# Kernel optimization log

Measured on AMD Instinct MI355X. Metric: run time of the kernel, lower is better.

The kernel has to match this reference:

```python
import jax, jax.numpy as jnp
import numpy as np
import math

D_MODEL = 1024
NUM_HEADS = 16
D_FF = 4096
EPS = 1e-5


def _linear_params(key, fan_in, fan_out):
    # torch nn.Linear default init: U(-1/sqrt(fan_in), 1/sqrt(fan_in))
    k1, k2 = jax.random.split(key)
    bound = 1.0 / math.sqrt(fan_in)
    W = jax.random.uniform(k1, (fan_in, fan_out), jnp.float32, -bound, bound)
    b = jax.random.uniform(k2, (fan_out,), jnp.float32, -bound, bound)
    return W, b


def setup_inputs() -> dict:
    key = jax.random.key(0)
    keys = jax.random.split(key, 16)
    src = jax.random.normal(keys[0], (4, 2048, D_MODEL), jnp.float32)
    tgt = jax.random.normal(keys[1], (4, 2048, D_MODEL), jnp.float32)
    sa_wq, sa_bq = _linear_params(keys[2], D_MODEL, D_MODEL)
    sa_wk, sa_bk = _linear_params(keys[3], D_MODEL, D_MODEL)
    sa_wv, sa_bv = _linear_params(keys[4], D_MODEL, D_MODEL)
    sa_wo, sa_bo = _linear_params(keys[5], D_MODEL, D_MODEL)
    ca_wq, ca_bq = _linear_params(keys[6], D_MODEL, D_MODEL)
    ca_wk, ca_bk = _linear_params(keys[7], D_MODEL, D_MODEL)
    ca_wv, ca_bv = _linear_params(keys[8], D_MODEL, D_MODEL)
    ca_wo, ca_bo = _linear_params(keys[9], D_MODEL, D_MODEL)
    ff_w1, ff_b1 = _linear_params(keys[10], D_MODEL, D_FF)
    ff_w2, ff_b2 = _linear_params(keys[11], D_FF, D_MODEL)
    ones = jnp.ones((D_MODEL,), jnp.float32)
    zeros = jnp.zeros((D_MODEL,), jnp.float32)
    return dict(
        src=src, tgt=tgt,
        sa_wq=sa_wq, sa_bq=sa_bq, sa_wk=sa_wk, sa_bk=sa_bk,
        sa_wv=sa_wv, sa_bv=sa_bv, sa_wo=sa_wo, sa_bo=sa_bo,
        ca_wq=ca_wq, ca_bq=ca_bq, ca_wk=ca_wk, ca_bk=ca_bk,
        ca_wv=ca_wv, ca_bv=ca_bv, ca_wo=ca_wo, ca_bo=ca_bo,
        ff_w1=ff_w1, ff_b1=ff_b1, ff_w2=ff_w2, ff_b2=ff_b2,
        ln1_g=ones, ln1_b=zeros, ln2_g=ones, ln2_b=zeros,
        ln3_g=ones, ln3_b=zeros,
    )


def _layernorm(x, g, b):
    mu = jnp.mean(x, axis=-1, keepdims=True)
    var = jnp.mean((x - mu) ** 2, axis=-1, keepdims=True)
    return (x - mu) * jax.lax.rsqrt(var + EPS) * g + b


def _mha(q_in, kv_in, wq, bq, wk, bk, wv, bv, wo, bo):
    B, Sq, D = q_in.shape
    Skv = kv_in.shape[1]
    H, dk = NUM_HEADS, D // NUM_HEADS
    Q = (q_in @ wq + bq).reshape(B, Sq, H, dk).transpose(0, 2, 1, 3)
    K = (kv_in @ wk + bk).reshape(B, Skv, H, dk).transpose(0, 2, 1, 3)
    V = (kv_in @ wv + bv).reshape(B, Skv, H, dk).transpose(0, 2, 1, 3)
    scores = jnp.einsum('bhqd,bhkd->bhqk', Q, K) / math.sqrt(dk)
    probs = jax.nn.softmax(scores, axis=-1)
    attn = jnp.einsum('bhqk,bhkd->bhqd', probs, V)
    attn = attn.transpose(0, 2, 1, 3).reshape(B, Sq, D)
    return attn @ wo + bo


def reference(src, tgt,
              sa_wq, sa_bq, sa_wk, sa_bk, sa_wv, sa_bv, sa_wo, sa_bo,
              ca_wq, ca_bq, ca_wk, ca_bk, ca_wv, ca_bv, ca_wo, ca_bo,
              ff_w1, ff_b1, ff_w2, ff_b2,
              ln1_g, ln1_b, ln2_g, ln2_b, ln3_g, ln3_b):
    # self-attention on tgt (dropout = identity in eval)
    sa = _mha(tgt, tgt, sa_wq, sa_bq, sa_wk, sa_bk, sa_wv, sa_bv, sa_wo, sa_bo)
    x = _layernorm(tgt + sa, ln1_g, ln1_b)
    # cross-attention: queries from decoder, keys/values from src
    ca = _mha(x, src, ca_wq, ca_bq, ca_wk, ca_bk, ca_wv, ca_bv, ca_wo, ca_bo)
    x = _layernorm(x + ca, ln2_g, ln2_b)
    # feed-forward
    ff = jax.nn.relu(x @ ff_w1 + ff_b1) @ ff_w2 + ff_b2
    x = _layernorm(x + ff, ln3_g, ln3_b)
    return x
```

## Files before the change

kernel.cpp:

```cpp
#include <hip/hip_runtime.h>
#include <hip/hip_bf16.h>
#include <stdint.h>


typedef __bf16 bf16_t;
typedef __bf16 bf16x8 __attribute__((ext_vector_type(8)));
typedef __bf16 bf16x4 __attribute__((ext_vector_type(4)));
typedef float  f32x4  __attribute__((ext_vector_type(4)));
typedef short  s16x4  __attribute__((ext_vector_type(4)));

#define SEQ_    2048
#define BATCH_  4
#define DM_     1024
#define NH_     16
#define DK_     64
#define DFF_    4096
#define TOK_    (BATCH_*SEQ_)
#define BH_     (BATCH_*NH_)
#define HEADEL_ ((size_t)BH_*SEQ_*DK_)

#define QSCALE_ 0.18033688011112042f

#define MFMA_BF16(a,b,c) __builtin_amdgcn_mfma_f32_16x16x32_bf16((a),(b),(c),0,0,0)
#define MFMA16(a,b,c) __builtin_amdgcn_mfma_f32_16x16x16bf16_1k((a),(b),(c),0,0,0)

static __device__ __forceinline__ void gl_lds16(const void* g, void* l) {
  __builtin_amdgcn_global_load_lds(
      (const __attribute__((address_space(1))) uint32_t*)g,
      (__attribute__((address_space(3))) uint32_t*)l, 16, 0, 0);
}

static __device__ __forceinline__ float fast_exp2(float x) {
#if __has_builtin(__builtin_amdgcn_exp2f)
  return __builtin_amdgcn_exp2f(x);
#else
  return exp2f(x);
#endif
}

__global__ __launch_bounds__(256) void cvt_bf16(const float* __restrict__ in,
                                                bf16_t* __restrict__ out, int n4) {
  int i = blockIdx.x * 256 + threadIdx.x;
  if (i < n4) {
    f32x4 v = *(const f32x4*)(in + (size_t)i * 4);
    bf16x4 o;
    o[0] = (bf16_t)v[0]; o[1] = (bf16_t)v[1]; o[2] = (bf16_t)v[2]; o[3] = (bf16_t)v[3];
    *(bf16x4*)(out + (size_t)i * 4) = o;
  }
}

__global__ __launch_bounds__(256) void transpose_w(const float* __restrict__ W,
                                                   bf16_t* __restrict__ Wt,
                                                   int K, int N) {
  __shared__ float t[32][33];
  int bx = blockIdx.x * 32;
  int by = blockIdx.y * 32;
  int tx = threadIdx.x;
  int ty = threadIdx.y;
  #pragma unroll
  for (int i = 0; i < 32; i += 8)
    t[ty + i][tx] = W[(size_t)(by + ty + i) * N + bx + tx];
  __syncthreads();
  #pragma unroll
  for (int i = 0; i < 32; i += 8)
    Wt[(size_t)(bx + ty + i) * K + by + tx] = (bf16_t)t[tx][ty + i];
}

__global__ __launch_bounds__(256) void gemm_bf16(
    const bf16_t* __restrict__ A, const bf16_t* __restrict__ Bt,
    const float* __restrict__ bias, const float* __restrict__ bias2,
    const float* __restrict__ bias3,
    float* outF, bf16_t* outB,
    int M, int N, int K, int mode, int relu, float scale)
{
  __shared__ __attribute__((aligned(16))) bf16_t lsA[2][128 * 32];
  __shared__ __attribute__((aligned(16))) bf16_t lsB[2][128 * 32];

  const int tid  = threadIdx.x;
  const int lane = tid & 63;
  const int w    = tid >> 6;
  const int q    = lane >> 4;
  const int r    = lane & 15;

  const int gx = gridDim.x;
  const int b  = blockIdx.y * gx + blockIdx.x;
  const int t_ = b >> 3;
  const int bm = (t_ / gx) * 8 + (b & 7);
  const int bn = t_ % gx;
  const int m0 = bm * 128;
  const int n0 = bn * 128;

  const int mb   = (w >> 1) * 64;
  const int nb   = (w & 1) * 64;

  f32x4 acc[4][4] = {};

  const int srow = tid >> 3;
  const int scol = (tid & 7) * 8 + 0;

  for (int k0 = 0; k0 < K; k0 += 64) {
    #pragma unroll
    for (int h = 0; h < 2; ++h) {
      #pragma unroll
      for (int rr = 0; rr < 2; ++rr) {
        int flat = rr * 2048 + tid * 8;
        int row = flat >> 5, col = flat & 31;
        gl_lds16(A  + (size_t)(m0 + row) * K + k0 + 32 * h + col, &lsA[h][flat]);
        gl_lds16(Bt + (size_t)(n0 + row) * K + k0 + 32 * h + col, &lsB[h][flat]);
      }
    }
    __syncthreads();
    #pragma unroll
    for (int h = 0; h < 2; ++h) {
      bf16x8 af[4], bfr[4];
      #pragma unroll
      for (int mi = 0; mi < 4; ++mi)
        af[mi] = *(const bf16x8*)&lsA[h][(mb + mi * 16 + r) * 32 + q * 8];
      #pragma unroll
      for (int ni = 0; ni < 4; ++ni)
        bfr[ni] = *(const bf16x8*)&lsB[h][(nb + ni * 16 + r) * 32 + q * 8];
      #pragma unroll
      for (int mi = 0; mi < 4; ++mi)
        #pragma unroll
        for (int ni = 0; ni < 4; ++ni)
          acc[mi][ni] = MFMA_BF16(af[mi], bfr[ni], acc[mi][ni]);
    }
    __syncthreads();
  }

  #pragma unroll
  for (int mi = 0; mi < 4; ++mi) {
    #pragma unroll
    for (int ni = 0; ni < 4; ++ni) {
      int col = n0 + nb + ni * 16 + r;
      float bv, sc = scale;
      int seg = 0, cw = col;
      if (mode == 3) {
        seg = col >> 10; cw = col & 1023;
        bv = (seg == 0) ? bias[cw] : ((seg == 1) ? bias2[cw] : bias3[cw]);
        if (seg != 0) sc = 1.f;
      } else if (mode == 4) {
        seg = col >> 10; cw = col & 1023;
        bv = (seg == 0) ? bias[cw] : bias2[cw];
      } else {
        bv = bias[col];
      }
      #pragma unroll
      for (int i = 0; i < 4; ++i) {
        int row = m0 + mb + mi * 16 + q * 4 + i;
        float v = (acc[mi][ni][i] + bv) * sc;
        if (relu) v = fmaxf(v, 0.f);
        if (outF) outF[(size_t)row * N + col] = v;
        if (outB) {
          size_t idx;
          if (mode == 0) {
            idx = (size_t)row * N + col;
          } else {
            int bb = row >> 11, s = row & 2047, h = cw >> 6, d = cw & 63;
            bool vt;
            size_t base;
            if (mode == 1)      { vt = false; base = 0; }
            else if (mode == 2) { vt = true;  base = 0; }
            else if (mode == 3) { vt = (seg == 2); base = (size_t)seg * HEADEL_; }
            else                { vt = (seg == 1); base = (size_t)seg * HEADEL_; }
            if (!vt) idx = base + ((size_t)(bb * NH_ + h) * SEQ_ + s) * DK_ + d;
            else     idx = base + ((size_t)(bb * NH_ + h) * DK_ + d) * SEQ_ + s;
          }
          outB[idx] = (bf16_t)v;
        }
      }
    }
  }
}

__global__ __launch_bounds__(256) void flash_attn(
    const bf16_t* __restrict__ Q, const bf16_t* __restrict__ Kb,
    const bf16_t* __restrict__ Vt, bf16_t* __restrict__ O)
{
  __shared__ __attribute__((aligned(16))) bf16_t Kls[64 * 64];
  __shared__ __attribute__((aligned(16))) bf16_t Vls[64 * 64];

  const int tid  = threadIdx.x;
  const int w    = tid >> 6;
  const int lane = tid & 63;
  const int q    = lane >> 4;
  const int r    = lane & 15;

  const int bl   = blockIdx.y * gridDim.x + blockIdx.x;
  const int bh   = (bl & 7) * 8 + ((bl >> 3) & 7);
  const int q0   = (bl >> 6) * 128 + w * 32;

  const bf16_t* Qp  = Q  + ((size_t)bh * SEQ_ + q0) * DK_;
  const bf16_t* Kp0 = Kb + (size_t)bh * SEQ_ * DK_;
  const bf16_t* Vp0 = Vt + (size_t)bh * DK_ * SEQ_;

  bf16x8 aq[2][2];
  #pragma unroll
  for (int rt = 0; rt < 2; ++rt)
    #pragma unroll
    for (int c = 0; c < 2; ++c)
      aq[rt][c] = *(const bf16x8*)(Qp + (rt * 16 + r) * DK_ + 32 * c + 8 * q);

  f32x4 o[2][4] = {};
  f32x4 l4[2] = {};

  const int srow0 = tid >> 3;
  const int scol0 = ((tid & 7) ^ (srow0 & 7)) * 8;
  const int srow1 = srow0 + 32;
  const int scol1 = ((tid & 7) ^ (srow1 & 7)) * 8;
  const int r7 = r & 7;

  for (int kv = 0; kv < SEQ_; kv += 64) {
    gl_lds16(Kp0 + (size_t)(kv + srow0) * DK_ + scol0, Kls + tid * 8);
    gl_lds16(Kp0 + (size_t)(kv + srow1) * DK_ + scol1, Kls + 2048 + tid * 8);
    gl_lds16(Vp0 + (size_t)srow0 * SEQ_ + kv + scol0, Vls + tid * 8);
    gl_lds16(Vp0 + (size_t)srow1 * SEQ_ + kv + scol1, Vls + 2048 + tid * 8);
    __syncthreads();

    bf16x8 kf[4][2];
    #pragma unroll
    for (int mt = 0; mt < 4; ++mt)
      #pragma unroll
      for (int c = 0; c < 2; ++c)
        kf[mt][c] = *(const bf16x8*)&Kls[(((16 * mt + r) * 8) + ((4 * c + q) ^ r7)) * 8];
    s16x4 vf[4][4];
    #pragma unroll
    for (int dt = 0; dt < 4; ++dt)
      #pragma unroll
      for (int mt = 0; mt < 4; ++mt)
        vf[dt][mt] = *(const s16x4*)&Vls[(((16 * dt + r) * 8) +
                        ((2 * mt + (q >> 1)) ^ r7)) * 8 + (q & 1) * 4];

    #pragma unroll
    for (int rt = 0; rt < 2; ++rt) {
      f32x4 st[4] = {};
      #pragma unroll
      for (int mt = 0; mt < 4; ++mt) {
        st[mt] = MFMA_BF16(kf[mt][0], aq[rt][0], st[mt]);
        st[mt] = MFMA_BF16(kf[mt][1], aq[rt][1], st[mt]);
      }
      s16x4 pf[4];
      f32x4 psum = {};
      #pragma unroll
      for (int mt = 0; mt < 4; ++mt) {
        f32x4 pe;
        #pragma unroll
        for (int i = 0; i < 4; ++i) pe[i] = fast_exp2(st[mt][i]);
        psum += pe;
        bf16x4 pb;
        #pragma unroll
        for (int i = 0; i < 4; ++i) pb[i] = (bf16_t)pe[i];
        pf[mt] = __builtin_bit_cast(s16x4, pb);
      }
      l4[rt] += psum;
      #pragma unroll
      for (int dt = 0; dt < 4; ++dt)
        #pragma unroll
        for (int mt = 0; mt < 4; ++mt)
          o[rt][dt] = MFMA16(vf[dt][mt], pf[mt], o[rt][dt]);
    }
    __syncthreads();
  }

  const int b = bh >> 4, h = bh & 15;
  #pragma unroll
  for (int rt = 0; rt < 2; ++rt) {
    float lr = (l4[rt][0] + l4[rt][1]) + (l4[rt][2] + l4[rt][3]);
    lr += __shfl_xor(lr, 16);
    lr += __shfl_xor(lr, 32);
    float linv = 1.f / lr;
    int token = b * SEQ_ + q0 + rt * 16 + r;
    #pragma unroll
    for (int dt = 0; dt < 4; ++dt) {
      bf16x4 ob;
      #pragma unroll
      for (int i = 0; i < 4; ++i) ob[i] = (bf16_t)(o[rt][dt][i] * linv);
      *(bf16x4*)(O + (size_t)token * DM_ + h * DK_ + 16 * dt + 4 * q) = ob;
    }
  }
}

__global__ __launch_bounds__(256) void resid_ln(
    const float* A, const float* Bv,
    const float* g, const float* be,
    float* outF, bf16_t* outB)
{
  const int w = threadIdx.x >> 6, lane = threadIdx.x & 63;
  const int row = blockIdx.x * 4 + w;
  const float* a = A  + (size_t)row * DM_;
  const float* b = Bv + (size_t)row * DM_;
  float v[16];
  float s = 0.f;
  #pragma unroll
  for (int c = 0; c < 4; ++c) {
    f32x4 x = *(const f32x4*)(a + c * 256 + lane * 4);
    f32x4 y = *(const f32x4*)(b + c * 256 + lane * 4);
    #pragma unroll
    for (int k = 0; k < 4; ++k) { v[c * 4 + k] = x[k] + y[k]; s += v[c * 4 + k]; }
  }
  s += __shfl_xor(s, 1);  s += __shfl_xor(s, 2);  s += __shfl_xor(s, 4);
  s += __shfl_xor(s, 8);  s += __shfl_xor(s, 16); s += __shfl_xor(s, 32);
  float mu = s * (1.f / DM_);
  float ss = 0.f;
  #pragma unroll
  for (int k = 0; k < 16; ++k) { float d = v[k] - mu; ss += d * d; }
  ss += __shfl_xor(ss, 1);  ss += __shfl_xor(ss, 2);  ss += __shfl_xor(ss, 4);
  ss += __shfl_xor(ss, 8);  ss += __shfl_xor(ss, 16); ss += __shfl_xor(ss, 32);
  float rstd = rsqrtf(ss * (1.f / DM_) + 1e-5f);
  #pragma unroll
  for (int c = 0; c < 4; ++c) {
    int idx = c * 256 + lane * 4;
    f32x4 gg = *(const f32x4*)(g + idx);
    f32x4 bb = *(const f32x4*)(be + idx);
    f32x4 ov; bf16x4 ob;
    #pragma unroll
    for (int k = 0; k < 4; ++k) {
      float val = (v[c * 4 + k] - mu) * rstd * gg[k] + bb[k];
      ov[k] = val; ob[k] = (bf16_t)val;
    }
    *(f32x4*)(outF + (size_t)row * DM_ + idx) = ov;
    if (outB) *(bf16x4*)(outB + (size_t)row * DM_ + idx) = ob;
  }
}

extern "C" void kernel_launch(void* const* d_in, const int* in_sizes, int n_in,
                              void* d_out, int out_size, void* d_ws, size_t ws_size,
                              hipStream_t stream)
{
  (void)in_sizes; (void)n_in; (void)out_size; (void)ws_size;
  const float* src   = (const float*)d_in[0];
  const float* tgt   = (const float*)d_in[1];
  const float* sa_wq = (const float*)d_in[2];  const float* sa_bq = (const float*)d_in[3];
  const float* sa_wk = (const float*)d_in[4];  const float* sa_bk = (const float*)d_in[5];
  const float* sa_wv = (const float*)d_in[6];  const float* sa_bv = (const float*)d_in[7];
  const float* sa_wo = (const float*)d_in[8];  const float* sa_bo = (const float*)d_in[9];
  const float* ca_wq = (const float*)d_in[10]; const float* ca_bq = (const float*)d_in[11];
  const float* ca_wk = (const float*)d_in[12]; const float* ca_bk = (const float*)d_in[13];
  const float* ca_wv = (const float*)d_in[14]; const float* ca_bv = (const float*)d_in[15];
  const float* ca_wo = (const float*)d_in[16]; const float* ca_bo = (const float*)d_in[17];
  const float* ff_w1 = (const float*)d_in[18]; const float* ff_b1 = (const float*)d_in[19];
  const float* ff_w2 = (const float*)d_in[20]; const float* ff_b2 = (const float*)d_in[21];
  const float* ln1g  = (const float*)d_in[22]; const float* ln1b  = (const float*)d_in[23];
  const float* ln2g  = (const float*)d_in[24]; const float* ln2b  = (const float*)d_in[25];
  const float* ln3g  = (const float*)d_in[26]; const float* ln3b  = (const float*)d_in[27];

  char* p = (char*)d_ws;
  auto alloc = [&](size_t bytes) -> char* {
    char* r = p; p += (bytes + 255) & ~(size_t)255; return r;
  };

  const size_t ACT_B  = (size_t)TOK_ * DM_ * 2;
  const size_t W_B    = (size_t)DM_ * DM_ * 2;
  const size_t HEAD_B = HEADEL_ * 2;

  bf16_t* tgt_bf = (bf16_t*)alloc(ACT_B);
  bf16_t* src_bf = (bf16_t*)alloc(ACT_B);
  bf16_t* wt_saq = (bf16_t*)alloc(W_B);
  bf16_t* wt_sak = (bf16_t*)alloc(W_B);
  bf16_t* wt_sav = (bf16_t*)alloc(W_B);
  bf16_t* wt_sao = (bf16_t*)alloc(W_B);
  bf16_t* wt_caq = (bf16_t*)alloc(W_B);
  bf16_t* wt_cak = (bf16_t*)alloc(W_B);
  bf16_t* wt_cav = (bf16_t*)alloc(W_B);
  bf16_t* wt_cao = (bf16_t*)alloc(W_B);
  bf16_t* w1t    = (bf16_t*)alloc((size_t)DFF_ * DM_ * 2);
  bf16_t* w2t    = (bf16_t*)alloc((size_t)DM_ * DFF_ * 2);
  char*   Rg     = alloc((size_t)TOK_ * DFF_ * 2);
  bf16_t* Qb     = (bf16_t*)Rg;
  bf16_t* Kbuf   = (bf16_t*)(Rg + HEAD_B);
  bf16_t* Vtb    = (bf16_t*)(Rg + 2 * HEAD_B);
  bf16_t* attnO  = (bf16_t*)(Rg + 3 * HEAD_B);
  bf16_t* hbuf   = (bf16_t*)Rg;
  float*  x1F    = (float*)alloc((size_t)TOK_ * DM_ * 4);
  bf16_t* x1B    = (bf16_t*)alloc(ACT_B);
  float*  x2F    = (float*)alloc((size_t)TOK_ * DM_ * 4);
  bf16_t* x2B    = (bf16_t*)alloc(ACT_B);
  float*  yF     = (float*)d_out;

  const int n4 = TOK_ * DM_ / 4;
  cvt_bf16<<<n4 / 256, 256, 0, stream>>>(tgt, tgt_bf, n4);
  cvt_bf16<<<n4 / 256, 256, 0, stream>>>(src, src_bf, n4);

  dim3 tb(32, 8);
  transpose_w<<<dim3(32, 32), tb, 0, stream>>>(sa_wq, wt_saq, DM_, DM_);
  transpose_w<<<dim3(32, 32), tb, 0, stream>>>(sa_wk, wt_sak, DM_, DM_);
  transpose_w<<<dim3(32, 32), tb, 0, stream>>>(sa_wv, wt_sav, DM_, DM_);
  transpose_w<<<dim3(32, 32), tb, 0, stream>>>(sa_wo, wt_sao, DM_, DM_);
  transpose_w<<<dim3(32, 32), tb, 0, stream>>>(ca_wq, wt_caq, DM_, DM_);
  transpose_w<<<dim3(32, 32), tb, 0, stream>>>(ca_wk, wt_cak, DM_, DM_);
  transpose_w<<<dim3(32, 32), tb, 0, stream>>>(ca_wv, wt_cav, DM_, DM_);
  transpose_w<<<dim3(32, 32), tb, 0, stream>>>(ca_wo, wt_cao, DM_, DM_);
  transpose_w<<<dim3(128, 32), tb, 0, stream>>>(ff_w1, w1t, DM_, DFF_);
  transpose_w<<<dim3(32, 128), tb, 0, stream>>>(ff_w2, w2t, DFF_, DM_);

  dim3 g1(DM_ / 128, TOK_ / 128);
  dim3 g3(3 * DM_ / 128, TOK_ / 128);
  dim3 g2(2 * DM_ / 128, TOK_ / 128);
  dim3 gf(DFF_ / 128, TOK_ / 128);
  dim3 ga(SEQ_ / 128, BH_);

  gemm_bf16<<<g3, 256, 0, stream>>>(tgt_bf, wt_saq, sa_bq, sa_bk, sa_bv,
                                    nullptr, Qb, TOK_, 3 * DM_, DM_, 3, 0, QSCALE_);
  flash_attn<<<ga, 256, 0, stream>>>(Qb, Kbuf, Vtb, attnO);
  gemm_bf16<<<g1, 256, 0, stream>>>(attnO, wt_sao, sa_bo, nullptr, nullptr,
                                    yF, nullptr, TOK_, DM_, DM_, 0, 0, 1.f);
  resid_ln<<<TOK_ / 4, 256, 0, stream>>>(tgt, yF, ln1g, ln1b, x1F, x1B);

  gemm_bf16<<<g1, 256, 0, stream>>>(x1B, wt_caq, ca_bq, nullptr, nullptr,
                                    nullptr, Qb, TOK_, DM_, DM_, 1, 0, QSCALE_);
  gemm_bf16<<<g2, 256, 0, stream>>>(src_bf, wt_cak, ca_bk, ca_bv, nullptr,
                                    nullptr, Kbuf, TOK_, 2 * DM_, DM_, 4, 0, 1.f);
  flash_attn<<<ga, 256, 0, stream>>>(Qb, Kbuf, Vtb, attnO);
  gemm_bf16<<<g1, 256, 0, stream>>>(attnO, wt_cao, ca_bo, nullptr, nullptr,
                                    yF, nullptr, TOK_, DM_, DM_, 0, 0, 1.f);
  resid_ln<<<TOK_ / 4, 256, 0, stream>>>(x1F, yF, ln2g, ln2b, x2F, x2B);

  gemm_bf16<<<gf, 256, 0, stream>>>(x2B, w1t, ff_b1, nullptr, nullptr,
                                    nullptr, hbuf, TOK_, DFF_, DM_, 0, 1, 1.f);
  gemm_bf16<<<g1, 256, 0, stream>>>(hbuf, w2t, ff_b2, nullptr, nullptr,
                                    yF, nullptr, TOK_, DM_, DFF_, 0, 0, 1.f);
  resid_ln<<<TOK_ / 4, 256, 0, stream>>>(x2F, yF, ln3g, ln3b, (float*)d_out, nullptr);
}
```

Baseline: 927.0 us.

## Double-buffer K/V tiles in flash attention and batch weight transposes

The flash attention kernel now uses two LDS buffers for K and V and issues the loads for the next tile before computing the current one. It waits with explicit vmcnt counts and raw barriers instead of full __syncthreads, and it raises wave priority around the MFMA blocks. Separately, the eight square weight transposes are merged into one launch using blockIdx.z, which assumes the destination buffers sit contiguously after wt_saq. The intent is to hide global-to-LDS latency behind compute and to cut launch overhead, at the cost of double the LDS per block, which may lower occupancy.

```diff
diff --git a/kernel.cpp b/kernel.cpp
--- a/kernel.cpp
+++ b/kernel.cpp
@@ -66,6 +66,36 @@
     Wt[(size_t)(bx + ty + i) * K + by + tx] = (bf16_t)t[tx][ty + i];
 }
 
+__global__ __launch_bounds__(256) void transpose_w8(
+    const float* __restrict__ w0, const float* __restrict__ w1,
+    const float* __restrict__ w2, const float* __restrict__ w3,
+    const float* __restrict__ w4, const float* __restrict__ w5,
+    const float* __restrict__ w6, const float* __restrict__ w7,
+    bf16_t* __restrict__ dst)
+{
+  __shared__ float t[32][33];
+  const int z = blockIdx.z;
+  const float* W;
+  switch (z) {
+    case 0: W = w0; break; case 1: W = w1; break;
+    case 2: W = w2; break; case 3: W = w3; break;
+    case 4: W = w4; break; case 5: W = w5; break;
+    case 6: W = w6; break; default: W = w7; break;
+  }
+  bf16_t* Wt = dst + (size_t)z * DM_ * DM_;
+  int bx = blockIdx.x * 32;
+  int by = blockIdx.y * 32;
+  int tx = threadIdx.x;
+  int ty = threadIdx.y;
+  #pragma unroll
+  for (int i = 0; i < 32; i += 8)
+    t[ty + i][tx] = W[(size_t)(by + ty + i) * DM_ + bx + tx];
+  __syncthreads();
+  #pragma unroll
+  for (int i = 0; i < 32; i += 8)
+    Wt[(size_t)(bx + ty + i) * DM_ + by + tx] = (bf16_t)t[tx][ty + i];
+}
+
 __global__ __launch_bounds__(256) void gemm_bf16(
     const bf16_t* __restrict__ A, const bf16_t* __restrict__ Bt,
     const float* __restrict__ bias, const float* __restrict__ bias2,
@@ -94,9 +124,6 @@
   const int nb   = (w & 1) * 64;
 
   f32x4 acc[4][4] = {};
-
-  const int srow = tid >> 3;
-  const int scol = (tid & 7) * 8 + 0;
 
   for (int k0 = 0; k0 < K; k0 += 64) {
     #pragma unroll
@@ -177,8 +204,8 @@
     const bf16_t* __restrict__ Q, const bf16_t* __restrict__ Kb,
     const bf16_t* __restrict__ Vt, bf16_t* __restrict__ O)
 {
-  __shared__ __attribute__((aligned(16))) bf16_t Kls[64 * 64];
-  __shared__ __attribute__((aligned(16))) bf16_t Vls[64 * 64];
+  __shared__ __attribute__((aligned(16))) bf16_t Kls[2][64 * 64];
+  __shared__ __attribute__((aligned(16))) bf16_t Vls[2][64 * 64];
 
   const int tid  = threadIdx.x;
   const int w    = tid >> 6;
@@ -201,44 +228,72 @@
     for (int c = 0; c < 2; ++c)
       aq[rt][c] = *(const bf16x8*)(Qp + (rt * 16 + r) * DK_ + 32 * c + 8 * q);
 
-  f32x4 o[2][4] = {};
-  f32x4 l4[2] = {};
-
   const int srow0 = tid >> 3;
   const int scol0 = ((tid & 7) ^ (srow0 & 7)) * 8;
   const int srow1 = srow0 + 32;
   const int scol1 = ((tid & 7) ^ (srow1 & 7)) * 8;
-  const int r7 = r & 7;
-
-  for (int kv = 0; kv < SEQ_; kv += 64) {
-    gl_lds16(Kp0 + (size_t)(kv + srow0) * DK_ + scol0, Kls + tid * 8);
-    gl_lds16(Kp0 + (size_t)(kv + srow1) * DK_ + scol1, Kls + 2048 + tid * 8);
-    gl_lds16(Vp0 + (size_t)srow0 * SEQ_ + kv + scol0, Vls + tid * 8);
-    gl_lds16(Vp0 + (size_t)srow1 * SEQ_ + kv + scol1, Vls + 2048 + tid * 8);
-    __syncthreads();
+  const int r7 = r & 15 & 7;
+
+#define STAGE_KV(bufi, kvoff) do {                                             \
+    gl_lds16(Kp0 + (size_t)((kvoff) + srow0) * DK_ + scol0,                    \
+             &Kls[bufi][tid * 8]);                                             \
+    gl_lds16(Kp0 + (size_t)((kvoff) + srow1) * DK_ + scol1,                    \
+             &Kls[bufi][2048 + tid * 8]);                                      \
+    gl_lds16(Vp0 + (size_t)srow0 * SEQ_ + (kvoff) + scol0,                     \
+             &Vls[bufi][tid * 8]);                                             \
+    gl_lds16(Vp0 + (size_t)srow1 * SEQ_ + (kvoff) + scol1,                     \
+             &Vls[bufi][2048 + tid * 8]);                                      \
+  } while (0)
+
+  STAGE_KV(0, 0);
+
+  #pragma unroll
+  for (int rt = 0; rt < 2; ++rt)
+    #pragma unroll
+    for (int c = 0; c < 2; ++c)
+      asm volatile("" :: "v"(__builtin_bit_cast(f32x4, aq[rt][c])));
+
+  f32x4 o[2][4] = {};
+  f32x4 l4[2] = {};
+  int cur = 0;
+
+  for (int t = 0; t < SEQ_ / 64; ++t) {
+    if (t < SEQ_ / 64 - 1) {
+      STAGE_KV(cur ^ 1, (t + 1) * 64);
+      asm volatile("s_waitcnt vmcnt(4)" ::: "memory");
+    } else {
+      asm volatile("s_waitcnt vmcnt(0)" ::: "memory");
+    }
+    __builtin_amdgcn_s_barrier();
+    __builtin_amdgcn_sched_barrier(0);
+
+    const bf16_t* KL = &Kls[cur][0];
+    const bf16_t* VL = &Vls[cur][0];
 
     bf16x8 kf[4][2];
     #pragma unroll
     for (int mt = 0; mt < 4; ++mt)
       #pragma unroll
       for (int c = 0; c < 2; ++c)
-        kf[mt][c] = *(const bf16x8*)&Kls[(((16 * mt + r) * 8) + ((4 * c + q) ^ r7)) * 8];
+        kf[mt][c] = *(const bf16x8*)&KL[(((16 * mt + r) * 8) + ((4 * c + q) ^ r7)) * 8];
     s16x4 vf[4][4];
     #pragma unroll
     for (int dt = 0; dt < 4; ++dt)
       #pragma unroll
       for (int mt = 0; mt < 4; ++mt)
-        vf[dt][mt] = *(const s16x4*)&Vls[(((16 * dt + r) * 8) +
+        vf[dt][mt] = *(const s16x4*)&VL[(((16 * dt + r) * 8) +
                         ((2 * mt + (q >> 1)) ^ r7)) * 8 + (q & 1) * 4];
 
     #pragma unroll
     for (int rt = 0; rt < 2; ++rt) {
       f32x4 st[4] = {};
+      __builtin_amdgcn_s_setprio(1);
       #pragma unroll
       for (int mt = 0; mt < 4; ++mt) {
         st[mt] = MFMA_BF16(kf[mt][0], aq[rt][0], st[mt]);
         st[mt] = MFMA_BF16(kf[mt][1], aq[rt][1], st[mt]);
       }
+      __builtin_amdgcn_s_setprio(0);
       s16x4 pf[4];
       f32x4 psum = {};
       #pragma unroll
@@ -253,14 +308,19 @@
         pf[mt] = __builtin_bit_cast(s16x4, pb);
       }
       l4[rt] += psum;
+      __builtin_amdgcn_s_setprio(1);
       #pragma unroll
       for (int dt = 0; dt < 4; ++dt)
         #pragma unroll
         for (int mt = 0; mt < 4; ++mt)
           o[rt][dt] = MFMA16(vf[dt][mt], pf[mt], o[rt][dt]);
-    }
-    __syncthreads();
-  }
+      __builtin_amdgcn_s_setprio(0);
+    }
+    __builtin_amdgcn_sched_barrier(0);
+    __builtin_amdgcn_s_barrier();
+    cur ^= 1;
+  }
+#undef STAGE_KV
 
   const int b = bh >> 4, h = bh & 15;
   #pragma unroll
@@ -382,14 +442,8 @@
   cvt_bf16<<<n4 / 256, 256, 0, stream>>>(src, src_bf, n4);
 
   dim3 tb(32, 8);
-  transpose_w<<<dim3(32, 32), tb, 0, stream>>>(sa_wq, wt_saq, DM_, DM_);
-  transpose_w<<<dim3(32, 32), tb, 0, stream>>>(sa_wk, wt_sak, DM_, DM_);
-  transpose_w<<<dim3(32, 32), tb, 0, stream>>>(sa_wv, wt_sav, DM_, DM_);
-  transpose_w<<<dim3(32, 32), tb, 0, stream>>>(sa_wo, wt_sao, DM_, DM_);
-  transpose_w<<<dim3(32, 32), tb, 0, stream>>>(ca_wq, wt_caq, DM_, DM_);
-  transpose_w<<<dim3(32, 32), tb, 0, stream>>>(ca_wk, wt_cak, DM_, DM_);
-  transpose_w<<<dim3(32, 32), tb, 0, stream>>>(ca_wv, wt_cav, DM_, DM_);
-  transpose_w<<<dim3(32, 32), tb, 0, stream>>>(ca_wo, wt_cao, DM_, DM_);
+  transpose_w8<<<dim3(32, 32, 8), tb, 0, stream>>>(
+      sa_wq, sa_wk, sa_wv, sa_wo, ca_wq, ca_wk, ca_wv, ca_wo, wt_saq);
   transpose_w<<<dim3(128, 32), tb, 0, stream>>>(ff_w1, w1t, DM_, DFF_);
   transpose_w<<<dim3(32, 128), tb, 0, stream>>>(ff_w2, w2t, DFF_, DM_);
 
```

New measurement: 985.7 us. 1.06x slower.

## Split-K the FFN down-projection and batch the eight attention weight transposes

Applied to the files above, without the earlier changes.

The FF2 GEMM (K=4096, only 512 output tiles) is split into two K halves that run as separate blocks. The second half writes its partial sums, without bias, into the now-free x1F buffer, and the final layernorm adds the three inputs. This doubles the number of blocks in the long-K GEMM to fill the GPU better, at the cost of writing and reading an extra fp32 activation tensor. The eight 1024x1024 weight transposes are also merged into one launch using a z-grid, which removes launch overhead.

```diff
diff --git a/kernel.cpp b/kernel.cpp
--- a/kernel.cpp
+++ b/kernel.cpp
@@ -66,12 +66,42 @@
     Wt[(size_t)(bx + ty + i) * K + by + tx] = (bf16_t)t[tx][ty + i];
 }
 
+__global__ __launch_bounds__(256) void transpose_w8(
+    const float* __restrict__ w0, const float* __restrict__ w1,
+    const float* __restrict__ w2, const float* __restrict__ w3,
+    const float* __restrict__ w4, const float* __restrict__ w5,
+    const float* __restrict__ w6, const float* __restrict__ w7,
+    bf16_t* __restrict__ dst)
+{
+  __shared__ float t[32][33];
+  const int z = blockIdx.z;
+  const float* W;
+  switch (z) {
+    case 0: W = w0; break; case 1: W = w1; break;
+    case 2: W = w2; break; case 3: W = w3; break;
+    case 4: W = w4; break; case 5: W = w5; break;
+    case 6: W = w6; break; default: W = w7; break;
+  }
+  bf16_t* Wt = dst + (size_t)z * DM_ * DM_;
+  int bx = blockIdx.x * 32;
+  int by = blockIdx.y * 32;
+  int tx = threadIdx.x;
+  int ty = threadIdx.y;
+  #pragma unroll
+  for (int i = 0; i < 32; i += 8)
+    t[ty + i][tx] = W[(size_t)(by + ty + i) * DM_ + bx + tx];
+  __syncthreads();
+  #pragma unroll
+  for (int i = 0; i < 32; i += 8)
+    Wt[(size_t)(bx + ty + i) * DM_ + by + tx] = (bf16_t)t[tx][ty + i];
+}
+
 __global__ __launch_bounds__(256) void gemm_bf16(
     const bf16_t* __restrict__ A, const bf16_t* __restrict__ Bt,
     const float* __restrict__ bias, const float* __restrict__ bias2,
     const float* __restrict__ bias3,
-    float* outF, bf16_t* outB,
-    int M, int N, int K, int mode, int relu, float scale)
+    float* outF, float* outF2, bf16_t* outB,
+    int M, int N, int K, int mode, int relu, float scale, int ksplit)
 {
   __shared__ __attribute__((aligned(16))) bf16_t lsA[2][128 * 32];
   __shared__ __attribute__((aligned(16))) bf16_t lsB[2][128 * 32];
@@ -85,8 +115,17 @@
   const int gx = gridDim.x;
   const int b  = blockIdx.y * gx + blockIdx.x;
   const int t_ = b >> 3;
-  const int bm = (t_ / gx) * 8 + (b & 7);
+  int bm = (t_ / gx) * 8 + (b & 7);
   const int bn = t_ % gx;
+
+  int kidx = 0;
+  int kbeg = 0, kend = K;
+  if (ksplit == 2) {
+    const int mtiles = M >> 7;
+    if (bm >= mtiles) { kidx = 1; bm -= mtiles; }
+    const int kh = K >> 1;
+    kbeg = kidx * kh; kend = kbeg + kh;
+  }
   const int m0 = bm * 128;
   const int n0 = bn * 128;
 
@@ -95,10 +134,7 @@
 
   f32x4 acc[4][4] = {};
 
-  const int srow = tid >> 3;
-  const int scol = (tid & 7) * 8 + 0;
-
-  for (int k0 = 0; k0 < K; k0 += 64) {
+  for (int k0 = kbeg; k0 < kend; k0 += 64) {
     #pragma unroll
     for (int h = 0; h < 2; ++h) {
       #pragma unroll
@@ -127,6 +163,8 @@
     }
     __syncthreads();
   }
+
+  float* ofp = kidx ? outF2 : outF;
 
   #pragma unroll
   for (int mi = 0; mi < 4; ++mi) {
@@ -145,12 +183,13 @@
       } else {
         bv = bias[col];
       }
+      if (kidx) bv = 0.f;
       #pragma unroll
       for (int i = 0; i < 4; ++i) {
         int row = m0 + mb + mi * 16 + q * 4 + i;
         float v = (acc[mi][ni][i] + bv) * sc;
         if (relu) v = fmaxf(v, 0.f);
-        if (outF) outF[(size_t)row * N + col] = v;
+        if (ofp) ofp[(size_t)row * N + col] = v;
         if (outB) {
           size_t idx;
           if (mode == 0) {
@@ -281,7 +320,7 @@
 }
 
 __global__ __launch_bounds__(256) void resid_ln(
-    const float* A, const float* Bv,
+    const float* A, const float* Bv, const float* Cv,
     const float* g, const float* be,
     float* outF, bf16_t* outB)
 {
@@ -289,14 +328,20 @@
   const int row = blockIdx.x * 4 + w;
   const float* a = A  + (size_t)row * DM_;
   const float* b = Bv + (size_t)row * DM_;
+  const float* c3 = Cv ? Cv + (size_t)row * DM_ : nullptr;
   float v[16];
   float s = 0.f;
   #pragma unroll
   for (int c = 0; c < 4; ++c) {
     f32x4 x = *(const f32x4*)(a + c * 256 + lane * 4);
     f32x4 y = *(const f32x4*)(b + c * 256 + lane * 4);
-    #pragma unroll
-    for (int k = 0; k < 4; ++k) { v[c * 4 + k] = x[k] + y[k]; s += v[c * 4 + k]; }
+    f32x4 z = {};
+    if (c3) z = *(const f32x4*)(c3 + c * 256 + lane * 4);
+    #pragma unroll
+    for (int k = 0; k < 4; ++k) {
+      v[c * 4 + k] = x[k] + y[k] + z[k];
+      s += v[c * 4 + k];
+    }
   }
   s += __shfl_xor(s, 1);  s += __shfl_xor(s, 2);  s += __shfl_xor(s, 4);
   s += __shfl_xor(s, 8);  s += __shfl_xor(s, 16); s += __shfl_xor(s, 32);
@@ -382,14 +427,8 @@
   cvt_bf16<<<n4 / 256, 256, 0, stream>>>(src, src_bf, n4);
 
   dim3 tb(32, 8);
-  transpose_w<<<dim3(32, 32), tb, 0, stream>>>(sa_wq, wt_saq, DM_, DM_);
-  transpose_w<<<dim3(32, 32), tb, 0, stream>>>(sa_wk, wt_sak, DM_, DM_);
-  transpose_w<<<dim3(32, 32), tb, 0, stream>>>(sa_wv, wt_sav, DM_, DM_);
-  transpose_w<<<dim3(32, 32), tb, 0, stream>>>(sa_wo, wt_sao, DM_, DM_);
-  transpose_w<<<dim3(32, 32), tb, 0, stream>>>(ca_wq, wt_caq, DM_, DM_);
-  transpose_w<<<dim3(32, 32), tb, 0, stream>>>(ca_wk, wt_cak, DM_, DM_);
-  transpose_w<<<dim3(32, 32), tb, 0, stream>>>(ca_wv, wt_cav, DM_, DM_);
-  transpose_w<<<dim3(32, 32), tb, 0, stream>>>(ca_wo, wt_cao, DM_, DM_);
+  transpose_w8<<<dim3(32, 32, 8), tb, 0, stream>>>(
+      sa_wq, sa_wk, sa_wv, sa_wo, ca_wq, ca_wk, ca_wv, ca_wo, wt_saq);
   transpose_w<<<dim3(128, 32), tb, 0, stream>>>(ff_w1, w1t, DM_, DFF_);
   transpose_w<<<dim3(32, 128), tb, 0, stream>>>(ff_w2, w2t, DFF_, DM_);
 
@@ -397,27 +436,36 @@
   dim3 g3(3 * DM_ / 128, TOK_ / 128);
   dim3 g2(2 * DM_ / 128, TOK_ / 128);
   dim3 gf(DFF_ / 128, TOK_ / 128);
+  dim3 gs(DM_ / 128, 2 * TOK_ / 128);
   dim3 ga(SEQ_ / 128, BH_);
 
   gemm_bf16<<<g3, 256, 0, stream>>>(tgt_bf, wt_saq, sa_bq, sa_bk, sa_bv,
-                                    nullptr, Qb, TOK_, 3 * DM_, DM_, 3, 0, QSCALE_);
+                                    nullptr, nullptr, Qb,
+                                    TOK_, 3 * DM_, DM_, 3, 0, QSCALE_, 1);
   flash_attn<<<ga, 256, 0, stream>>>(Qb, Kbuf, Vtb, attnO);
   gemm_bf16<<<g1, 256, 0, stream>>>(attnO, wt_sao, sa_bo, nullptr, nullptr,
-                                    yF, nullptr, TOK_, DM_, DM_, 0, 0, 1.f);
-  resid_ln<<<TOK_ / 4, 256, 0, stream>>>(tgt, yF, ln1g, ln1b, x1F, x1B);
+                                    yF, nullptr, nullptr,
+                                    TOK_, DM_, DM_, 0, 0, 1.f, 1);
+  resid_ln<<<TOK_ / 4, 256, 0, stream>>>(tgt, yF, nullptr, ln1g, ln1b, x1F, x1B);
 
   gemm_bf16<<<g1, 256, 0, stream>>>(x1B, wt_caq, ca_bq, nullptr, nullptr,
-                                    nullptr, Qb, TOK_, DM_, DM_, 1, 0, QSCALE_);
+                                    nullptr, nullptr, Qb,
+                                    TOK_, DM_, DM_, 1, 0, QSCALE_, 1);
   gemm_bf16<<<g2, 256, 0, stream>>>(src_bf, wt_cak, ca_bk, ca_bv, nullptr,
-                                    nullptr, Kbuf, TOK_, 2 * DM_, DM_, 4, 0, 1.f);
+                                    nullptr, nullptr, Kbuf,
+                                    TOK_, 2 * DM_, DM_, 4, 0, 1.f, 1);
   flash_attn<<<ga, 256, 0, stream>>>(Qb, Kbuf, Vtb, attnO);
   gemm_bf16<<<g1, 256, 0, stream>>>(attnO, wt_cao, ca_bo, nullptr, nullptr,
-                                    yF, nullptr, TOK_, DM_, DM_, 0, 0, 1.f);
-  resid_ln<<<TOK_ / 4, 256, 0, stream>>>(x1F, yF, ln2g, ln2b, x2F, x2B);
+                                    yF, nullptr, nullptr,
+                                    TOK_, DM_, DM_, 0, 0, 1.f, 1);
+  resid_ln<<<TOK_ / 4, 256, 0, stream>>>(x1F, yF, nullptr, ln2g, ln2b, x2F, x2B);
 
   gemm_bf16<<<gf, 256, 0, stream>>>(x2B, w1t, ff_b1, nullptr, nullptr,
-                                    nullptr, hbuf, TOK_, DFF_, DM_, 0, 1, 1.f);
-  gemm_bf16<<<g1, 256, 0, stream>>>(hbuf, w2t, ff_b2, nullptr, nullptr,
-                                    yF, nullptr, TOK_, DM_, DFF_, 0, 0, 1.f);
-  resid_ln<<<TOK_ / 4, 256, 0, stream>>>(x2F, yF, ln3g, ln3b, (float*)d_out, nullptr);
-}
+                                    nullptr, nullptr, hbuf,
+                                    TOK_, DFF_, DM_, 0, 1, 1.f, 1);
+  gemm_bf16<<<gs, 256, 0, stream>>>(hbuf, w2t, ff_b2, nullptr, nullptr,
+                                    yF, x1F, nullptr,
+                                    TOK_, DM_, DFF_, 0, 0, 1.f, 2);
+  resid_ln<<<TOK_ / 4, 256, 0, stream>>>(x2F, yF, x1F,
+                                         ln3g, ln3b, (float*)d_out, nullptr);
+}
```

Measured after the change: 968.0 us. 4.4% more time.
